# Performance work log

Hardware: AMD Instinct MI355X
Metric: run time of the kernel (lower is better)

## Reference

```python
import jax, jax.numpy as jnp
import numpy as np

B, S, H, K, L, NH, FF = 4, 2048, 2048, 1024, 2, 16, 4096
EPS = 1e-5

def _alibi_slopes(n):
    # standard power-of-two ALiBi slopes
    start = 2.0 ** (-8.0 / n)
    return start ** jnp.arange(1, n + 1, dtype=jnp.float32)

def _layernorm(h, g, b):
    mu = jnp.mean(h, axis=-1, keepdims=True)
    var = jnp.mean(jnp.square(h - mu), axis=-1, keepdims=True)
    return (h - mu) * jax.lax.rsqrt(var + EPS) * g + b

def setup_inputs() -> dict:
    key = jax.random.key(0)
    ks = jax.random.split(key, 16)
    x = jax.random.normal(ks[0], (B, S, H), jnp.float32)
    prev = jax.random.normal(ks[1], (B, S, H), jnp.float32)
    # unique sorted token indices per batch row (jit-friendly boolean mask)
    idx = jnp.stack([jnp.sort(jax.random.permutation(jax.random.fold_in(ks[2], b), S)[:K])
                     for b in range(B)]).astype(jnp.int32)
    w = 0.02
    Wq = jax.random.normal(ks[3], (L, H, H), jnp.float32) * w
    Wk = jax.random.normal(ks[4], (L, H, H), jnp.float32) * w
    Wv = jax.random.normal(ks[5], (L, H, H), jnp.float32) * w
    Wo = jax.random.normal(ks[6], (L, H, H), jnp.float32) * w
    attn_gamma = jnp.ones((L, H), jnp.float32)
    attn_beta = jnp.zeros((L, H), jnp.float32)
    mlp_gamma = jnp.ones((L, H), jnp.float32)
    mlp_beta = jnp.zeros((L, H), jnp.float32)
    Wgate = jax.random.normal(ks[7], (L, H, FF), jnp.float32) * w
    Wup = jax.random.normal(ks[8], (L, H, FF), jnp.float32) * w
    Wdown = jax.random.normal(ks[9], (L, FF, H), jnp.float32) * w
    return {"x": x, "prev": prev, "idx": idx, "Wq": Wq, "Wk": Wk, "Wv": Wv,
            "Wo": Wo, "attn_gamma": attn_gamma, "attn_beta": attn_beta,
            "mlp_gamma": mlp_gamma, "mlp_beta": mlp_beta,
            "Wgate": Wgate, "Wup": Wup, "Wdown": Wdown}

def _forward(x, prev, idx, Wq, Wk, Wv, Wo, attn_gamma, attn_beta,
             mlp_gamma, mlp_beta, Wgate, Wup, Wdown):
    d = H // NH
    scale = 1.0 / jnp.sqrt(jnp.asarray(d, jnp.float32))
    # gather selected tokens: [B, K, H]
    cur = jnp.take_along_axis(x, idx[:, :, None], axis=1)
    mem = jnp.take_along_axis(prev, idx[:, :, None], axis=1)
    # non-causal ALiBi bias over selected-sequence positions: [NH, K, K]
    pos = jnp.arange(K)
    dist = jnp.abs(pos[:, None] - pos[None, :]).astype(jnp.float32)
    bias = -_alibi_slopes(NH)[:, None, None] * dist
    for l in range(L):
        q = (cur @ Wq[l]).reshape(B, K, NH, d)
        k = (mem @ Wk[l]).reshape(B, K, NH, d)
        v = (mem @ Wv[l]).reshape(B, K, NH, d)
        scores = jnp.einsum('bqhd,bkhd->bhqk', q, k) * scale + bias
        attn = jax.nn.softmax(scores, axis=-1)
        o = jnp.einsum('bhqk,bkhd->bqhd', attn, v).reshape(B, K, H) @ Wo[l]
        cur = cur + o
        normed = _layernorm(cur, attn_gamma[l], attn_beta[l])
        mlp = (jax.nn.silu(normed @ Wgate[l]) * (normed @ Wup[l])) @ Wdown[l]
        cur = cur + mlp
        cur = _layernorm(cur, mlp_gamma[l], mlp_beta[l])
    # scatter-add back: out[mask] += update_val
    out = x.at[jnp.arange(B)[:, None], idx].add(cur)
    return out

def reference(x, prev, idx, Wq, Wk, Wv, Wo, attn_gamma, attn_beta,
              mlp_gamma, mlp_beta, Wgate, Wup, Wdown):
    return _forward(x, prev, idx, Wq, Wk, Wv, Wo, attn_gamma, attn_beta,
                    mlp_gamma, mlp_beta, Wgate, Wup, Wdown)
```

## Files before the change

kernel.cpp:

```cpp
#include <hip/hip_runtime.h>
#include <hip/hip_bf16.h>

#define BB 4
#define SS 2048
#define HH 2048
#define KK 1024
#define LL 2
#define NHH 16
#define FFF 4096
#define DD 128

typedef __attribute__((ext_vector_type(8))) short s8v;
typedef __attribute__((ext_vector_type(4))) short s4v;
typedef __attribute__((ext_vector_type(4))) float f4v;

__device__ __forceinline__ short f2bf(float f) {
  unsigned u = __builtin_bit_cast(unsigned, f);
  u += 0x7fffu + ((u >> 16) & 1u);
  return (short)(u >> 16);
}
__device__ __forceinline__ float bf2f(short s) {
  unsigned u = ((unsigned)(unsigned short)s) << 16;
  return __builtin_bit_cast(float, u);
}
__device__ __forceinline__ f4v mfma16(s8v a, s8v b, f4v c) {
  asm("v_mfma_f32_16x16x32_bf16 %0, %1, %2, %0" : "+v"(c) : "v"(a), "v"(b));
  return c;
}
__device__ __forceinline__ void gload_lds16(const void* g, void* l) {
  __builtin_amdgcn_global_load_lds(
      (__attribute__((address_space(1))) void*)g,
      (__attribute__((address_space(3))) void*)l, 16, 0, 0);
}

__global__ __launch_bounds__(256) void wconv(const float* __restrict__ W,
                                             short* __restrict__ Wt,
                                             int Kd, int N) {
  __shared__ short tile[64][65];
  int n0 = blockIdx.x * 64, k0 = blockIdx.y * 64;
  int t = threadIdx.x;
#pragma unroll
  for (int i = 0; i < 16; ++i) {
    int lin = i * 256 + t;
    int r = lin >> 6, c = lin & 63;
    tile[c][r] = f2bf(W[(size_t)(k0 + r) * N + n0 + c]);
  }
  __syncthreads();
#pragma unroll
  for (int i = 0; i < 16; ++i) {
    int lin = i * 256 + t;
    int r = lin >> 6, c = lin & 63;
    Wt[(size_t)(n0 + r) * Kd + k0 + c] = tile[r][c];
  }
}

__global__ __launch_bounds__(256) void gather_rows(
    const float* __restrict__ x, const float* __restrict__ prev,
    const int* __restrict__ idx, float* __restrict__ cur_f,
    short* __restrict__ cur_b, short* __restrict__ mem_b) {
  int r = blockIdx.x;
  int b = r >> 10, kk = r & (KK - 1);
  int src = idx[b * KK + kk];
  const float4* xs = (const float4*)(x + ((size_t)b * SS + src) * HH);
  const float4* ps = (const float4*)(prev + ((size_t)b * SS + src) * HH);
  float4* cf = (float4*)(cur_f + (size_t)r * HH);
  s4v* cb = (s4v*)(cur_b + (size_t)r * HH);
  s4v* mb = (s4v*)(mem_b + (size_t)r * HH);
  int t = threadIdx.x;
#pragma unroll
  for (int i = 0; i < 2; ++i) {
    int c = t + i * 256;
    float4 xv = xs[c], pv = ps[c];
    cf[c] = xv;
    s4v cv, mv;
    cv[0] = f2bf(xv.x); cv[1] = f2bf(xv.y); cv[2] = f2bf(xv.z); cv[3] = f2bf(xv.w);
    mv[0] = f2bf(pv.x); mv[1] = f2bf(pv.y); mv[2] = f2bf(pv.z); mv[3] = f2bf(pv.w);
    cb[c] = cv; mb[c] = mv;
  }
}

template <int EPI>
__global__ __launch_bounds__(512, 2) void g8p(
    const short* __restrict__ A, const short* __restrict__ Bt,
    float* __restrict__ Cf, short* __restrict__ Cb,
    const short* __restrict__ Other, int M, int N, int Kd) {
  __shared__ __align__(16) short smem[2 * 12288];
  const int t = threadIdx.x;
  const int w = t >> 6, l = t & 63;
  const int wr = w >> 2, wc = w & 3;
  const int l15 = l & 15, lh = l >> 4;
  const int koff = lh * 8;

  const int gx = gridDim.x, gy = gridDim.y;
  const int nwg = gx * gy;
  const int bid = blockIdx.y * gx + blockIdx.x;
  const int wg = (bid & 7) * (nwg >> 3) + (bid >> 3);
  const int by = wg & (gy - 1);
  const int bx = wg / gy;
  const int rowBase = by * 128, colBase = bx * 256;

  const int ar = t >> 2, ac = (t & 3) * 8;
  const short* gA = A + (size_t)(rowBase + ar) * Kd + ac;
  const short* gB0 = Bt + (size_t)(colBase + ar) * Kd + ac;
  const short* gB1 = gB0 + (size_t)128 * Kd;
  short* lA = smem + t * 8;
  short* lB = smem + 4096 + t * 8;

  f4v acc[4][4];
#pragma unroll
  for (int i = 0; i < 4; ++i)
#pragma unroll
    for (int j = 0; j < 4; ++j) acc[i][j] = (f4v){0.f, 0.f, 0.f, 0.f};

  const int NT = Kd >> 5;
  gload_lds16(gA, lA);
  gload_lds16(gB0, lB);
  gload_lds16(gB1, lB + 4096);
  __syncthreads();

  for (int kt = 0; kt < NT; ++kt) {
    const short* sb = smem + (kt & 1) * 12288;
    if (kt + 1 < NT) {
      const int k0 = (kt + 1) * 32;
      const int o = ((kt & 1) ^ 1) * 12288;
      gload_lds16(gA + k0, lA + o);
      gload_lds16(gB0 + k0, lB + o);
      gload_lds16(gB1 + k0, lB + o + 4096);
    }
    s8v af[4], bf[4];
#pragma unroll
    for (int mt = 0; mt < 4; ++mt)
      af[mt] = *(const s8v*)(sb + (wr * 64 + mt * 16 + l15) * 32 + koff);
#pragma unroll
    for (int nt = 0; nt < 4; ++nt)
      bf[nt] = *(const s8v*)(sb + 4096 + (wc * 64 + nt * 16 + l15) * 32 + koff);
#pragma unroll
    for (int mt = 0; mt < 4; ++mt)
#pragma unroll
      for (int nt = 0; nt < 4; ++nt)
        acc[mt][nt] = mfma16(af[mt], bf[nt], acc[mt][nt]);
    __syncthreads();
  }

#pragma unroll
  for (int mt = 0; mt < 4; ++mt) {
#pragma unroll
    for (int nt = 0; nt < 4; ++nt) {
#pragma unroll
      for (int rr = 0; rr < 4; ++rr) {
        int row = rowBase + wr * 64 + mt * 16 + lh * 4 + rr;
        int col = colBase + wc * 64 + nt * 16 + l15;
        float v = acc[mt][nt][rr];
        if constexpr (EPI == 0) {
          Cb[(size_t)row * N + col] = f2bf(v);
        } else if constexpr (EPI == 1) {
          Cf[(size_t)row * N + col] += v;
        } else if constexpr (EPI == 2) {
          int b = row >> 10, ktok = row & (KK - 1);
          int h = col >> 7, dd = col & (DD - 1);
          Cb[(((size_t)(b * NHH + h)) * DD + dd) * KK + ktok] = f2bf(v);
        } else if constexpr (EPI == 3) {
          float sv = v / (1.f + __expf(-v));
          Cb[(size_t)row * N + col] = f2bf(sv);
        } else {
          float o = bf2f(Other[(size_t)row * N + col]);
          Cb[(size_t)row * N + col] = f2bf(v * o);
        }
      }
    }
  }
}

__global__ __launch_bounds__(256, 2) void attn_fwd(
    const short* __restrict__ qb, const short* __restrict__ kb,
    const short* __restrict__ vT, short* __restrict__ ob) {
  __shared__ __align__(16) short Kl[64 * 136];
  __shared__ __align__(16) short Vl[128 * 72];
  __shared__ __align__(16) short Pl[64 * 72];
  int b = blockIdx.z, h = blockIdx.y, qt = blockIdx.x;
  int t = threadIdx.x, w = t >> 6, l = t & 63, l15 = l & 15, lh = l >> 4;
  float slope = exp2f(-0.5f * (float)(h + 1));
  const float scale = 0.08838834764831845f;

  s8v qf[4];
  int qrowA = qt * 64 + w * 16 + l15;
  const short* qptr = qb + ((size_t)(b * KK + qrowA)) * HH + h * DD + lh * 8;
#pragma unroll
  for (int ks = 0; ks < 4; ++ks) qf[ks] = *(const s8v*)(qptr + ks * 32);

  f4v oacc[8];
#pragma unroll
  for (int i = 0; i < 8; ++i) oacc[i] = (f4v){0.f, 0.f, 0.f, 0.f};
  float m[4], sden[4];
#pragma unroll
  for (int r = 0; r < 4; ++r) { m[r] = -1e30f; sden[r] = 0.f; }
  int qpos_base = qt * 64 + w * 16 + lh * 4;

  for (int kt = 0; kt < KK / 64; ++kt) {
    {
      int rr = t >> 4, cc = (t & 15) * 8;
#pragma unroll
      for (int it = 0; it < 4; ++it) {
        int krow = it * 16 + rr;
        s8v g = *(const s8v*)(kb + ((size_t)(b * KK + kt * 64 + krow)) * HH + h * DD + cc);
        *(s8v*)&Kl[krow * 136 + cc] = g;
      }
      int dr = t >> 3, c2 = (t & 7) * 8;
#pragma unroll
      for (int it = 0; it < 4; ++it) {
        int drow = it * 32 + dr;
        s8v g = *(const s8v*)(vT + (((size_t)(b * NHH + h)) * DD + drow) * KK + kt * 64 + c2);
        *(s8v*)&Vl[drow * 72 + c2] = g;
      }
    }
    __syncthreads();

    f4v sacc[4];
#pragma unroll
    for (int ct = 0; ct < 4; ++ct) sacc[ct] = (f4v){0.f, 0.f, 0.f, 0.f};
#pragma unroll
    for (int ct = 0; ct < 4; ++ct)
#pragma unroll
      for (int ks = 0; ks < 4; ++ks) {
        s8v kf = *(const s8v*)&Kl[(ct * 16 + l15) * 136 + ks * 32 + lh * 8];
        sacc[ct] = mfma16(qf[ks], kf, sacc[ct]);
      }

#pragma unroll
    for (int r = 0; r < 4; ++r) {
      int qpos = qpos_base + r;
      float mx = -1e30f;
#pragma unroll
      for (int ct = 0; ct < 4; ++ct) {
        int kpos = kt * 64 + ct * 16 + l15;
        float sv = sacc[ct][r] * scale - slope * fabsf((float)(qpos - kpos));
        sacc[ct][r] = sv;
        mx = fmaxf(mx, sv);
      }
      mx = fmaxf(mx, __shfl_xor(mx, 1));
      mx = fmaxf(mx, __shfl_xor(mx, 2));
      mx = fmaxf(mx, __shfl_xor(mx, 4));
      mx = fmaxf(mx, __shfl_xor(mx, 8));
      float mn = fmaxf(m[r], mx);
      float corr = __expf(m[r] - mn);
      m[r] = mn;
      float ps = 0.f;
#pragma unroll
      for (int ct = 0; ct < 4; ++ct) {
        float p = __expf(sacc[ct][r] - mn);
        sacc[ct][r] = p;
        ps += p;
      }
      ps += __shfl_xor(ps, 1); ps += __shfl_xor(ps, 2);
      ps += __shfl_xor(ps, 4); ps += __shfl_xor(ps, 8);
      sden[r] = sden[r] * corr + ps;
#pragma unroll
      for (int dt = 0; dt < 8; ++dt) oacc[dt][r] *= corr;
#pragma unroll
      for (int ct = 0; ct < 4; ++ct)
        Pl[(w * 16 + lh * 4 + r) * 72 + ct * 16 + l15] = f2bf(sacc[ct][r]);
    }

#pragma unroll
    for (int ks2 = 0; ks2 < 2; ++ks2) {
      s8v pa = *(const s8v*)&Pl[(w * 16 + l15) * 72 + ks2 * 32 + lh * 8];
#pragma unroll
      for (int dt = 0; dt < 8; ++dt) {
        s8v vf = *(const s8v*)&Vl[(dt * 16 + l15) * 72 + ks2 * 32 + lh * 8];
        oacc[dt] = mfma16(pa, vf, oacc[dt]);
      }
    }
    __syncthreads();
  }

#pragma unroll
  for (int dt = 0; dt < 8; ++dt)
#pragma unroll
    for (int r = 0; r < 4; ++r) {
      int qpos = qpos_base + r;
      int dd = dt * 16 + l15;
      ob[((size_t)(b * KK + qpos)) * HH + h * DD + dd] = f2bf(oacc[dt][r] / sden[r]);
    }
}

__global__ __launch_bounds__(256) void ln_rows(const float* in,
    const float* __restrict__ gma, const float* __restrict__ bta,
    short* __restrict__ outb, float* outf) {
  __shared__ float red[2][4];
  int r = blockIdx.x, t = threadIdx.x;
  const float4* x4 = (const float4*)(in + (size_t)r * HH);
  float4 va = x4[t], vb = x4[t + 256];
  float sum = va.x + va.y + va.z + va.w + vb.x + vb.y + vb.z + vb.w;
  float sq = va.x * va.x + va.y * va.y + va.z * va.z + va.w * va.w +
             vb.x * vb.x + vb.y * vb.y + vb.z * vb.z + vb.w * vb.w;
#pragma unroll
  for (int off = 32; off; off >>= 1) {
    sum += __shfl_down(sum, off);
    sq += __shfl_down(sq, off);
  }
  int w = t >> 6;
  if ((t & 63) == 0) { red[0][w] = sum; red[1][w] = sq; }
  __syncthreads();
  sum = red[0][0] + red[0][1] + red[0][2] + red[0][3];
  sq = red[1][0] + red[1][1] + red[1][2] + red[1][3];
  float mu = sum * (1.f / HH);
  float rs = rsqrtf(sq * (1.f / HH) - mu * mu + 1e-5f);
  const float4* g4 = (const float4*)gma;
  const float4* b4 = (const float4*)bta;
  s4v* ob = (s4v*)(outb + (size_t)r * HH);
  float4* of = (float4*)(outf ? outf + (size_t)r * HH : nullptr);
#pragma unroll
  for (int i = 0; i < 2; ++i) {
    int c = t + i * 256;
    float4 v = (i == 0) ? va : vb;
    float4 g = g4[c], bb = b4[c];
    float4 nv;
    nv.x = (v.x - mu) * rs * g.x + bb.x;
    nv.y = (v.y - mu) * rs * g.y + bb.y;
    nv.z = (v.z - mu) * rs * g.z + bb.z;
    nv.w = (v.w - mu) * rs * g.w + bb.w;
    s4v o;
    o[0] = f2bf(nv.x); o[1] = f2bf(nv.y); o[2] = f2bf(nv.z); o[3] = f2bf(nv.w);
    ob[c] = o;
    if (outf) of[c] = nv;
  }
}

__global__ __launch_bounds__(256) void copy_out(const float* __restrict__ x,
                                                float* __restrict__ out, size_t n4) {
  size_t i = (size_t)blockIdx.x * 256 + threadIdx.x;
  size_t stride = (size_t)gridDim.x * 256;
  const float4* xi = (const float4*)x;
  float4* oi = (float4*)out;
  for (; i < n4; i += stride) oi[i] = xi[i];
}

__global__ __launch_bounds__(256) void scatter_add(const int* __restrict__ idx,
                                                   const float* __restrict__ cur,
                                                   float* out) {
  int r = blockIdx.x;
  int b = r >> 10, kk = r & (KK - 1);
  int dst = idx[b * KK + kk];
  float4* o = (float4*)(out + ((size_t)b * SS + dst) * HH);
  const float4* c = (const float4*)(cur + (size_t)r * HH);
  int t = threadIdx.x;
#pragma unroll
  for (int i = 0; i < 2; ++i) {
    int j = t + i * 256;
    float4 ov = o[j], cv = c[j];
    ov.x += cv.x; ov.y += cv.y; ov.z += cv.z; ov.w += cv.w;
    o[j] = ov;
  }
}

extern "C" void kernel_launch(void* const* d_in, const int* in_sizes, int n_in,
                              void* d_out, int out_size, void* d_ws, size_t ws_size,
                              hipStream_t stream) {
  (void)in_sizes; (void)n_in; (void)out_size; (void)ws_size;
  const float* x = (const float*)d_in[0];
  const float* prv = (const float*)d_in[1];
  const int* idx = (const int*)d_in[2];
  const float* Wq = (const float*)d_in[3];
  const float* Wk = (const float*)d_in[4];
  const float* Wv = (const float*)d_in[5];
  const float* Wo = (const float*)d_in[6];
  const float* ag = (const float*)d_in[7];
  const float* ab = (const float*)d_in[8];
  const float* mg = (const float*)d_in[9];
  const float* mbt = (const float*)d_in[10];
  const float* Wg = (const float*)d_in[11];
  const float* Wu = (const float*)d_in[12];
  const float* Wd = (const float*)d_in[13];
  float* out = (float*)d_out;

  char* ws = (char*)d_ws;
  size_t off = 0;
  auto alloc = [&](size_t bytes) -> void* {
    void* p = ws + off;
    off += (bytes + 255) & ~(size_t)255;
    return p;
  };
  const size_t WHH = (size_t)HH * HH, WHF = (size_t)HH * FFF;
  short* WqT = (short*)alloc(LL * WHH * 2);
  short* WkT = (short*)alloc(LL * WHH * 2);
  short* WvT = (short*)alloc(LL * WHH * 2);
  short* WoT = (short*)alloc(LL * WHH * 2);
  short* WgT = (short*)alloc(LL * WHF * 2);
  short* WuT = (short*)alloc(LL * WHF * 2);
  short* WdT = (short*)alloc(LL * WHF * 2);
  const size_t RH = (size_t)BB * KK * HH;
  float* cur_f = (float*)alloc(RH * 4);
  short* q_b = (short*)alloc(RH * 2);
  short* k_b = (short*)alloc(RH * 2);
  short* vT_b = (short*)alloc(RH * 2);
  short* o_b = (short*)alloc(RH * 2);
  short* cur_b = (short*)alloc(RH * 2);
  short* mem_b = (short*)alloc(RH * 2);
  short* nrm_b = (short*)alloc(RH * 2);
  short* sg_b = q_b;
  short* hid_b = vT_b;

  dim3 blk(256), blk512(512);
  for (int l = 0; l < LL; ++l) {
    wconv<<<dim3(HH / 64, HH / 64), blk, 0, stream>>>(Wq + l * WHH, WqT + l * WHH, HH, HH);
    wconv<<<dim3(HH / 64, HH / 64), blk, 0, stream>>>(Wk + l * WHH, WkT + l * WHH, HH, HH);
    wconv<<<dim3(HH / 64, HH / 64), blk, 0, stream>>>(Wv + l * WHH, WvT + l * WHH, HH, HH);
    wconv<<<dim3(HH / 64, HH / 64), blk, 0, stream>>>(Wo + l * WHH, WoT + l * WHH, HH, HH);
    wconv<<<dim3(FFF / 64, HH / 64), blk, 0, stream>>>(Wg + l * WHF, WgT + l * WHF, HH, FFF);
    wconv<<<dim3(FFF / 64, HH / 64), blk, 0, stream>>>(Wu + l * WHF, WuT + l * WHF, HH, FFF);
    wconv<<<dim3(HH / 64, FFF / 64), blk, 0, stream>>>(Wd + l * WHF, WdT + l * WHF, FFF, HH);
  }
  gather_rows<<<dim3(BB * KK), blk, 0, stream>>>(x, prv, idx, cur_f, cur_b, mem_b);

  const int M = BB * KK;
  for (int l = 0; l < LL; ++l) {
    const short* wq = WqT + l * WHH;
    const short* wk = WkT + l * WHH;
    const short* wv = WvT + l * WHH;
    const short* wo = WoT + l * WHH;
    const short* wg_ = WgT + l * WHF;
    const short* wu = WuT + l * WHF;
    const short* wd = WdT + l * WHF;
    g8p<0><<<dim3(HH / 256, M / 128), blk512, 0, stream>>>(cur_b, wq, nullptr, q_b, nullptr, M, HH, HH);
    g8p<0><<<dim3(HH / 256, M / 128), blk512, 0, stream>>>(mem_b, wk, nullptr, k_b, nullptr, M, HH, HH);
    g8p<2><<<dim3(HH / 256, M / 128), blk512, 0, stream>>>(mem_b, wv, nullptr, vT_b, nullptr, M, HH, HH);
    attn_fwd<<<dim3(KK / 64, NHH, BB), blk, 0, stream>>>(q_b, k_b, vT_b, o_b);
    g8p<1><<<dim3(HH / 256, M / 128), blk512, 0, stream>>>(o_b, wo, cur_f, nullptr, nullptr, M, HH, HH);
    ln_rows<<<dim3(M), blk, 0, stream>>>(cur_f, ag + l * HH, ab + l * HH, nrm_b, nullptr);
    g8p<3><<<dim3(FFF / 256, M / 128), blk512, 0, stream>>>(nrm_b, wg_, nullptr, sg_b, nullptr, M, FFF, HH);
    g8p<4><<<dim3(FFF / 256, M / 128), blk512, 0, stream>>>(nrm_b, wu, nullptr, hid_b, sg_b, M, FFF, HH);
    g8p<1><<<dim3(HH / 256, M / 128), blk512, 0, stream>>>(hid_b, wd, cur_f, nullptr, nullptr, M, HH, FFF);
    ln_rows<<<dim3(M), blk, 0, stream>>>(cur_f, mg + l * HH, mbt + l * HH, cur_b, cur_f);
  }
  copy_out<<<dim3(2048), blk, 0, stream>>>(x, out, (size_t)BB * SS * HH / 4);
  scatter_add<<<dim3(M), blk, 0, stream>>>(idx, cur_f, out);
}
```

Measured before the change: 1.447 ms.

## Switch GEMMs to 4-wave blocks with templated column tile width

Replaces the 8-wave 128x256 GEMM kernel with a 4-wave kernel templated on tile width. The HxH projections use 128x128 tiles, which doubles the grid to 512 blocks for better CU fill. The FFN gate/up projections use 128x256 tiles, so each wave holds a 64x128 accumulator for more MFMA work per LDS read. The cost is more register pressure in the wide variant and less per-block reuse in the narrow one.

```diff
diff --git a/kernel.cpp b/kernel.cpp
--- a/kernel.cpp
+++ b/kernel.cpp
@@ -79,15 +79,19 @@
   }
 }
 
-template <int EPI>
-__global__ __launch_bounds__(512, 2) void g8p(
+template <int TN, int EPI>
+__global__ __launch_bounds__(256, 2) void g2(
     const short* __restrict__ A, const short* __restrict__ Bt,
     float* __restrict__ Cf, short* __restrict__ Cb,
     const short* __restrict__ Other, int M, int N, int Kd) {
-  __shared__ __align__(16) short smem[2 * 12288];
+  constexpr int NFB = TN / 32;
+  constexpr int BSH = TN * 32;
+  constexpr int BUFS = 4096 + BSH;
+  constexpr int NLB = TN / 64;
+  __shared__ __align__(16) short smem[2 * BUFS];
   const int t = threadIdx.x;
   const int w = t >> 6, l = t & 63;
-  const int wr = w >> 2, wc = w & 3;
+  const int wr = w >> 1, wc = w & 1;
   const int l15 = l & 15, lh = l >> 4;
   const int koff = lh * 8;
 
@@ -97,47 +101,52 @@
   const int wg = (bid & 7) * (nwg >> 3) + (bid >> 3);
   const int by = wg & (gy - 1);
   const int bx = wg / gy;
-  const int rowBase = by * 128, colBase = bx * 256;
-
-  const int ar = t >> 2, ac = (t & 3) * 8;
-  const short* gA = A + (size_t)(rowBase + ar) * Kd + ac;
-  const short* gB0 = Bt + (size_t)(colBase + ar) * Kd + ac;
-  const short* gB1 = gB0 + (size_t)128 * Kd;
+  const int rowBase = by * 128, colBase = bx * TN;
+
+  const int sr = t >> 2, sc = (t & 3) * 8;
+  const short* gA = A + (size_t)(rowBase + sr) * Kd + sc;
+  const short* gB = Bt + (size_t)(colBase + sr) * Kd + sc;
   short* lA = smem + t * 8;
   short* lB = smem + 4096 + t * 8;
 
-  f4v acc[4][4];
+  f4v acc[4][NFB];
 #pragma unroll
   for (int i = 0; i < 4; ++i)
 #pragma unroll
-    for (int j = 0; j < 4; ++j) acc[i][j] = (f4v){0.f, 0.f, 0.f, 0.f};
+    for (int j = 0; j < NFB; ++j) acc[i][j] = (f4v){0.f, 0.f, 0.f, 0.f};
 
   const int NT = Kd >> 5;
-  gload_lds16(gA, lA);
-  gload_lds16(gB0, lB);
-  gload_lds16(gB1, lB + 4096);
+  {
+    gload_lds16(gA, lA);
+    gload_lds16(gA + (size_t)64 * Kd, lA + 2048);
+#pragma unroll
+    for (int i = 0; i < NLB; ++i)
+      gload_lds16(gB + (size_t)(i * 64) * Kd, lB + i * 2048);
+  }
   __syncthreads();
 
   for (int kt = 0; kt < NT; ++kt) {
-    const short* sb = smem + (kt & 1) * 12288;
+    const short* sb = smem + (kt & 1) * BUFS;
     if (kt + 1 < NT) {
       const int k0 = (kt + 1) * 32;
-      const int o = ((kt & 1) ^ 1) * 12288;
+      const int o = ((kt & 1) ^ 1) * BUFS;
       gload_lds16(gA + k0, lA + o);
-      gload_lds16(gB0 + k0, lB + o);
-      gload_lds16(gB1 + k0, lB + o + 4096);
-    }
-    s8v af[4], bf[4];
+      gload_lds16(gA + k0 + (size_t)64 * Kd, lA + o + 2048);
+#pragma unroll
+      for (int i = 0; i < NLB; ++i)
+        gload_lds16(gB + k0 + (size_t)(i * 64) * Kd, lB + o + i * 2048);
+    }
+    s8v af[4], bf[NFB];
 #pragma unroll
     for (int mt = 0; mt < 4; ++mt)
       af[mt] = *(const s8v*)(sb + (wr * 64 + mt * 16 + l15) * 32 + koff);
 #pragma unroll
-    for (int nt = 0; nt < 4; ++nt)
-      bf[nt] = *(const s8v*)(sb + 4096 + (wc * 64 + nt * 16 + l15) * 32 + koff);
+    for (int nt = 0; nt < NFB; ++nt)
+      bf[nt] = *(const s8v*)(sb + 4096 + (wc * (TN / 2) + nt * 16 + l15) * 32 + koff);
 #pragma unroll
     for (int mt = 0; mt < 4; ++mt)
 #pragma unroll
-      for (int nt = 0; nt < 4; ++nt)
+      for (int nt = 0; nt < NFB; ++nt)
         acc[mt][nt] = mfma16(af[mt], bf[nt], acc[mt][nt]);
     __syncthreads();
   }
@@ -145,11 +154,11 @@
 #pragma unroll
   for (int mt = 0; mt < 4; ++mt) {
 #pragma unroll
-    for (int nt = 0; nt < 4; ++nt) {
+    for (int nt = 0; nt < NFB; ++nt) {
 #pragma unroll
       for (int rr = 0; rr < 4; ++rr) {
         int row = rowBase + wr * 64 + mt * 16 + lh * 4 + rr;
-        int col = colBase + wc * 64 + nt * 16 + l15;
+        int col = colBase + wc * (TN / 2) + nt * 16 + l15;
         float v = acc[mt][nt][rr];
         if constexpr (EPI == 0) {
           Cb[(size_t)row * N + col] = f2bf(v);
@@ -400,7 +409,7 @@
   short* sg_b = q_b;
   short* hid_b = vT_b;
 
-  dim3 blk(256), blk512(512);
+  dim3 blk(256);
   for (int l = 0; l < LL; ++l) {
     wconv<<<dim3(HH / 64, HH / 64), blk, 0, stream>>>(Wq + l * WHH, WqT + l * WHH, HH, HH);
     wconv<<<dim3(HH / 64, HH / 64), blk, 0, stream>>>(Wk + l * WHH, WkT + l * WHH, HH, HH);
@@ -421,15 +430,15 @@
     const short* wg_ = WgT + l * WHF;
     const short* wu = WuT + l * WHF;
     const short* wd = WdT + l * WHF;
-    g8p<0><<<dim3(HH / 256, M / 128), blk512, 0, stream>>>(cur_b, wq, nullptr, q_b, nullptr, M, HH, HH);
-    g8p<0><<<dim3(HH / 256, M / 128), blk512, 0, stream>>>(mem_b, wk, nullptr, k_b, nullptr, M, HH, HH);
-    g8p<2><<<dim3(HH / 256, M / 128), blk512, 0, stream>>>(mem_b, wv, nullptr, vT_b, nullptr, M, HH, HH);
+    g2<128, 0><<<dim3(HH / 128, M / 128), blk, 0, stream>>>(cur_b, wq, nullptr, q_b, nullptr, M, HH, HH);
+    g2<128, 0><<<dim3(HH / 128, M / 128), blk, 0, stream>>>(mem_b, wk, nullptr, k_b, nullptr, M, HH, HH);
+    g2<128, 2><<<dim3(HH / 128, M / 128), blk, 0, stream>>>(mem_b, wv, nullptr, vT_b, nullptr, M, HH, HH);
     attn_fwd<<<dim3(KK / 64, NHH, BB), blk, 0, stream>>>(q_b, k_b, vT_b, o_b);
-    g8p<1><<<dim3(HH / 256, M / 128), blk512, 0, stream>>>(o_b, wo, cur_f, nullptr, nullptr, M, HH, HH);
+    g2<128, 1><<<dim3(HH / 128, M / 128), blk, 0, stream>>>(o_b, wo, cur_f, nullptr, nullptr, M, HH, HH);
     ln_rows<<<dim3(M), blk, 0, stream>>>(cur_f, ag + l * HH, ab + l * HH, nrm_b, nullptr);
-    g8p<3><<<dim3(FFF / 256, M / 128), blk512, 0, stream>>>(nrm_b, wg_, nullptr, sg_b, nullptr, M, FFF, HH);
-    g8p<4><<<dim3(FFF / 256, M / 128), blk512, 0, stream>>>(nrm_b, wu, nullptr, hid_b, sg_b, M, FFF, HH);
-    g8p<1><<<dim3(HH / 256, M / 128), blk512, 0, stream>>>(hid_b, wd, cur_f, nullptr, nullptr, M, HH, FFF);
+    g2<256, 3><<<dim3(FFF / 256, M / 128), blk, 0, stream>>>(nrm_b, wg_, nullptr, sg_b, nullptr, M, FFF, HH);
+    g2<256, 4><<<dim3(FFF / 256, M / 128), blk, 0, stream>>>(nrm_b, wu, nullptr, hid_b, sg_b, M, FFF, HH);
+    g2<128, 1><<<dim3(HH / 128, M / 128), blk, 0, stream>>>(hid_b, wd, cur_f, nullptr, nullptr, M, HH, FFF);
     ln_rows<<<dim3(M), blk, 0, stream>>>(cur_f, mg + l * HH, mbt + l * HH, cur_b, cur_f);
   }
   copy_out<<<dim3(2048), blk, 0, stream>>>(x, out, (size_t)BB * SS * HH / 4);
```

After: 1.510 ms. 1.04x slower.

## Triple-buffer GEMM LDS staging with partial vmcnt waits

Applied to the files above, without the earlier changes.

The bf16 MFMA GEMM kernel moves from double to triple buffering of its A/B tiles in shared memory, prefetching two k-steps ahead. The barrier now uses a custom s_waitcnt vmcnt(3), so only the older stage's loads must land before threads sync, leaving the newest prefetch in flight. This is meant to hide global load latency behind MFMA work. It raises LDS use from 48KB to 72KB per block, which may limit the two-blocks-per-CU occupancy target.

```diff
diff --git a/kernel.cpp b/kernel.cpp
--- a/kernel.cpp
+++ b/kernel.cpp
@@ -31,6 +31,15 @@
   __builtin_amdgcn_global_load_lds(
       (__attribute__((address_space(1))) void*)g,
       (__attribute__((address_space(3))) void*)l, 16, 0, 0);
+}
+template <int N>
+__device__ __forceinline__ void barrier_cnt() {
+  if constexpr (N == 3)
+    asm volatile("s_waitcnt vmcnt(3) expcnt(0) lgkmcnt(0)" ::: "memory");
+  else
+    asm volatile("s_waitcnt vmcnt(0) expcnt(0) lgkmcnt(0)" ::: "memory");
+  __builtin_amdgcn_s_barrier();
+  asm volatile("" ::: "memory");
 }
 
 __global__ __launch_bounds__(256) void wconv(const float* __restrict__ W,
@@ -84,7 +93,7 @@
     const short* __restrict__ A, const short* __restrict__ Bt,
     float* __restrict__ Cf, short* __restrict__ Cb,
     const short* __restrict__ Other, int M, int N, int Kd) {
-  __shared__ __align__(16) short smem[2 * 12288];
+  __shared__ __align__(16) short smem[3 * 12288];
   const int t = threadIdx.x;
   const int w = t >> 6, l = t & 63;
   const int wr = w >> 2, wc = w & 3;
@@ -103,8 +112,16 @@
   const short* gA = A + (size_t)(rowBase + ar) * Kd + ac;
   const short* gB0 = Bt + (size_t)(colBase + ar) * Kd + ac;
   const short* gB1 = gB0 + (size_t)128 * Kd;
-  short* lA = smem + t * 8;
-  short* lB = smem + 4096 + t * 8;
+  const int lA = t * 8;
+  const int lB = 4096 + t * 8;
+
+  auto stage = [&](int bi, int kt) {
+    const int k0 = kt * 32;
+    short* base = smem + bi * 12288;
+    gload_lds16(gA + k0, base + lA);
+    gload_lds16(gB0 + k0, base + lB);
+    gload_lds16(gB1 + k0, base + lB + 4096);
+  };
 
   f4v acc[4][4];
 #pragma unroll
@@ -113,19 +130,17 @@
     for (int j = 0; j < 4; ++j) acc[i][j] = (f4v){0.f, 0.f, 0.f, 0.f};
 
   const int NT = Kd >> 5;
-  gload_lds16(gA, lA);
-  gload_lds16(gB0, lB);
-  gload_lds16(gB1, lB + 4096);
-  __syncthreads();
-
+  stage(0, 0);
+  stage(1, 1);
+  barrier_cnt<3>();
+
+  int cur = 0;
   for (int kt = 0; kt < NT; ++kt) {
-    const short* sb = smem + (kt & 1) * 12288;
-    if (kt + 1 < NT) {
-      const int k0 = (kt + 1) * 32;
-      const int o = ((kt & 1) ^ 1) * 12288;
-      gload_lds16(gA + k0, lA + o);
-      gload_lds16(gB0 + k0, lB + o);
-      gload_lds16(gB1 + k0, lB + o + 4096);
+    const short* sb = smem + cur * 12288;
+    const bool more = (kt + 2 < NT);
+    if (more) {
+      int nb = cur + 2; if (nb >= 3) nb -= 3;
+      stage(nb, kt + 2);
     }
     s8v af[4], bf[4];
 #pragma unroll
@@ -139,7 +154,8 @@
 #pragma unroll
       for (int nt = 0; nt < 4; ++nt)
         acc[mt][nt] = mfma16(af[mt], bf[nt], acc[mt][nt]);
-    __syncthreads();
+    if (more) barrier_cnt<3>(); else barrier_cnt<0>();
+    cur = (cur + 1 == 3) ? 0 : cur + 1;
   }
 
 #pragma unroll
```

Result: faster. 1.342 ms (-7.3%).
